# Kernel optimization log

Measured on AMD Instinct MI355X. Metric: run time of the kernel, lower is better.

Reference implementation:

```python
import jax, jax.numpy as jnp
import numpy as np
from jax import lax

DN = ('NCHW', 'OIHW', 'NCHW')

def conv(x, w, groups=1):
    return lax.conv_general_dilated(x, w, (1, 1), 'SAME',
                                    feature_group_count=groups,
                                    dimension_numbers=DN)

def layernorm_cf(x, w, b, eps=1e-6):
    # channels-first LayerNorm over dim=1
    u = x.mean(1, keepdims=True)
    s = ((x - u) ** 2).mean(1, keepdims=True)
    xn = (x - u) / jnp.sqrt(s + eps)
    return w[None, :, None, None] * xn + b[None, :, None, None]

def l2norm(x, eps=1e-12):
    n = jnp.sqrt(jnp.sum(x * x, axis=-1, keepdims=True))
    return x / jnp.maximum(n, eps)

def setup_inputs() -> dict:
    key = jax.random.key(0)
    ks = jax.random.split(key, 16)
    B, C, H, W = 4, 192, 128, 128
    heads = 6
    hidden = int(C * 2.66)  # 510
    s = 0.02
    rn = lambda k, shp: jax.random.normal(k, shp, dtype=jnp.float32) * s
    return {
        'x': jax.random.normal(ks[0], (B, C, H, W), dtype=jnp.float32),
        'ln_w': jnp.ones((C,), jnp.float32),
        'ln_b': jnp.zeros((C,), jnp.float32),
        'temperature': jnp.ones((heads, 1, 1), jnp.float32),
        'q_w': rn(ks[1], (C, C, 1, 1)),
        'q_dw_w': rn(ks[2], (C, 1, 3, 3)),
        'kv_w': rn(ks[3], (2 * C, C, 1, 1)),
        'kv_dw_w': rn(ks[4], (2 * C, 1, 3, 3)),
        'proj_w': rn(ks[5], (C, C, 1, 1)),
        'pos_embed': rn(ks[6], (1, C, 1, 1)),
        'pos_q_w': rn(ks[7], (C, C, 1, 1)),
        'pos_k_w': rn(ks[8], (C, C, 1, 1)),
        'sel_in_w': rn(ks[9], (hidden, C, 3, 3)),
        'sel_dw_w': rn(ks[10], (hidden, 1, 3, 3)),
        'sel_out_w': rn(ks[11], (C, hidden, 3, 3)),
        'alpha': jnp.float32(0.5),
    }

def reference(x, ln_w, ln_b, temperature, q_w, q_dw_w, kv_w, kv_dw_w,
              proj_w, pos_embed, pos_q_w, pos_k_w,
              sel_in_w, sel_dw_w, sel_out_w, alpha):
    b, c, h, w = x.shape
    heads = temperature.shape[0]
    ch = c // heads
    n = h * w

    # --- CFA on norm_x (norm_x == norm_y since both are norm(x)) ---
    norm_x = layernorm_cf(x, ln_w, ln_b)
    q = conv(conv(norm_x, q_w), q_dw_w, groups=c)
    kv = conv(conv(norm_x, kv_w), kv_dw_w, groups=2 * c)
    k, v = jnp.split(kv, 2, axis=1)

    q = q.reshape(b, heads, ch, n)
    k = k.reshape(b, heads, ch, n)
    v = v.reshape(b, heads, ch, n)

    qn = l2norm(q)
    kn = l2norm(k)
    attn = jax.nn.softmax(jnp.einsum('bhcn,bhdn->bhcd', qn, kn) * temperature[None], axis=-1)
    out = jnp.einsum('bhcd,bhdn->bhcn', attn, v)

    pos_x = norm_x + pos_embed
    pos_q = conv(pos_x, pos_q_w).reshape(b, heads, ch, n)
    pos_k = conv(pos_x, pos_k_w).reshape(b, heads, ch, n)
    pos_attn = jax.nn.softmax(jnp.einsum('bhcn,bhdn->bhcd', pos_q, pos_k), axis=-1)
    pos_out = jnp.einsum('bhcd,bhdn->bhcn', pos_attn, v)

    out = (out + pos_out).reshape(b, c, h, w)
    out = conv(out, proj_w)
    x = x + alpha * out

    # --- SEL (conv-FFN) ---
    nx = layernorm_cf(x, ln_w, ln_b)
    g = conv(nx, sel_in_w)
    g = conv(g, sel_dw_w, groups=g.shape[1])
    g = jax.nn.silu(g)
    g = conv(g, sel_out_w)
    x = x + (1.0 - alpha) * g
    return x
```

## Files before the change

kernel.cpp:

```cpp
#include <hip/hip_runtime.h>
#include <hip/hip_bf16.h>
#include <stdint.h>

#define DEVI __device__ __forceinline__

typedef __attribute__((ext_vector_type(8))) unsigned short us8;
typedef __attribute__((ext_vector_type(4))) unsigned short us4;
typedef __attribute__((ext_vector_type(8))) __bf16 bf16x8;
typedef __attribute__((ext_vector_type(4))) float f32x4;

#define BB 4
#define CC 192
#define HH 128
#define NPIX 16384
#define MTOT 65536
#define HEADS 6

DEVI float b2f(unsigned short u){ return __uint_as_float(((unsigned)u)<<16); }
DEVI unsigned short f2b(float f){
  unsigned u = __float_as_uint(f);
  return (unsigned short)((u + 0x7fffu + ((u>>16)&1u)) >> 16);
}

DEVI void gload16(const void* g, void* l){
  __builtin_amdgcn_global_load_lds((const __attribute__((address_space(1))) unsigned int*)g,
                                   (__attribute__((address_space(3))) unsigned int*)l,
                                   16, 0, 0);
}

__global__ __launch_bounds__(256)
void ln1_k(const float* __restrict__ x, const float* __restrict__ lnw,
           const float* __restrict__ lnb, unsigned short* __restrict__ nx)
{
  __shared__ float tile[CC*65];
  __shared__ float stats[64*2];
  int gbase = blockIdx.x * 64;
  int b = gbase >> 14; int n0 = gbase & (NPIX-1);
  for (int idx = threadIdx.x; idx < CC*64; idx += 256){
    int c = idx >> 6, j = idx & 63;
    tile[c*65 + j] = x[((size_t)b*CC + c)*NPIX + n0 + j];
  }
  __syncthreads();
  if (threadIdx.x < 64){
    int j = threadIdx.x;
    float s = 0.f, ss = 0.f;
    for (int c = 0; c < CC; c++){ float v = tile[c*65 + j]; s += v; ss += v*v; }
    float mu = s * (1.f/CC);
    float var = ss * (1.f/CC) - mu*mu;
    stats[j*2] = mu; stats[j*2+1] = rsqrtf(var + 1e-6f);
  }
  __syncthreads();
  for (int idx = threadIdx.x; idx < CC*64; idx += 256){
    int c = idx % CC, j = idx / CC;
    float v = (tile[c*65 + j] - stats[j*2]) * stats[j*2+1] * lnw[c] + lnb[c];
    nx[(size_t)(gbase + j)*CC + c] = f2b(v);
  }
}

__global__ __launch_bounds__(256)
void ln2_k(const float* __restrict__ x2, const float* __restrict__ lnw,
           const float* __restrict__ lnb, unsigned short* __restrict__ nx)
{
  int gm = blockIdx.x*4 + (threadIdx.x >> 6);
  int lane = threadIdx.x & 63;
  const float* row = x2 + (size_t)gm*CC;
  float v0 = row[lane], v1 = row[lane+64], v2 = row[lane+128];
  float s = v0+v1+v2, ss = v0*v0+v1*v1+v2*v2;
  #pragma unroll
  for (int o = 32; o >= 1; o >>= 1){
    s  += __shfl_xor(s,  o);
    ss += __shfl_xor(ss, o);
  }
  float mu = s * (1.f/CC);
  float rstd = rsqrtf(ss*(1.f/CC) - mu*mu + 1e-6f);
  unsigned short* o0 = nx + (size_t)gm*CC;
  o0[lane]     = f2b((v0-mu)*rstd*lnw[lane]     + lnb[lane]);
  o0[lane+64]  = f2b((v1-mu)*rstd*lnw[lane+64]  + lnb[lane+64]);
  o0[lane+128] = f2b((v2-mu)*rstd*lnw[lane+128] + lnb[lane+128]);
}

template<int EPI, int NSLICES>
__global__ __launch_bounds__(512, 2)
void gemm256_k(const unsigned short* __restrict__ A, int strideA,
               const unsigned short* __restrict__ W, int Ktot,
               int NcolsW, int NcolsStore, int outStride, int colBlocks,
               unsigned short* __restrict__ outB,
               const float* __restrict__ res, float* __restrict__ outF,
               const float* __restrict__ alphaP,
               const unsigned short* __restrict__ zerop)
{
  __shared__ unsigned short lds[65536];

  const int tid = threadIdx.x;
  const int l  = tid & 63;
  const int w  = tid >> 6;
  const int wm = w >> 2;
  const int wn = w & 3;

  const int q8 = gridDim.x >> 3;
  const int bid = (blockIdx.x & 7)*q8 + (blockIdx.x >> 3);
  const int mblk = bid / colBlocks;
  const int nblk = bid - mblk*colBlocks;
  const int m0 = mblk*256, co0 = nblk*256;

  int rowT[4], slotX[4];
  #pragma unroll
  for (int i = 0; i < 4; i++){
    rowT[i]  = (w*4 + i)*8 + (l >> 3);
    slotX[i] = (l & 7) ^ (rowT[i] & 7);
  }
  const unsigned short* baseA[4];
  int hhA[4], wwA[4];
  #pragma unroll
  for (int i = 0; i < 4; i++){
    int gm = m0 + rowT[i];
    int np = gm & (NPIX-1);
    hhA[i] = np >> 7; wwA[i] = np & 127;
    baseA[i] = A + (size_t)gm*strideA + (slotX[i] << 3);
  }
  const unsigned short* baseB[4];
  bool bval[4];
  #pragma unroll
  for (int i = 0; i < 4; i++){
    int co = co0 + rowT[i];
    bval[i] = (co < NcolsW);
    baseB[i] = bval[i] ? (W + (size_t)co*Ktot + (slotX[i] << 3)) : (zerop + (l << 3));
  }

  const int NT = Ktot >> 6;

  auto STAGE = [&](int ts){
    int buf = ts & 1;
    unsigned short* la = lds + buf*16384;
    unsigned short* lb = lds + 32768 + buf*16384;
    int ci0, dy = 0, dx = 0;
    if constexpr (NSLICES == 1){ ci0 = ts << 6; }
    else { int cib = ts/9, s = ts - cib*9; ci0 = cib << 6; dy = s/3 - 1; dx = s - (s/3)*3 - 1; }
    #pragma unroll
    for (int i = 0; i < 4; i++){
      const unsigned short* srcA;
      if constexpr (NSLICES == 1){
        srcA = baseA[i] + ci0;
      } else {
        int h2 = hhA[i] + dy, w2 = wwA[i] + dx;
        srcA = ((unsigned)h2 < 128u && (unsigned)w2 < 128u)
             ? (baseA[i] + (dy*HH + dx)*strideA + ci0)
             : (zerop + (l << 3));
      }
      gload16(srcA, la + (w*4 + i)*512);
    }
    #pragma unroll
    for (int i = 0; i < 4; i++){
      const unsigned short* srcB = bval[i] ? (baseB[i] + (ts << 6)) : baseB[i];
      gload16(srcB, lb + (w*4 + i)*512);
    }
  };

  f32x4 acc[8][4] = {};

  STAGE(0);
  for (int t = 0; t < NT; ++t){
    if (t + 1 < NT){
      STAGE(t + 1);
      asm volatile("s_waitcnt vmcnt(8)" ::: "memory");
    } else {
      asm volatile("s_waitcnt vmcnt(0)" ::: "memory");
    }
    __builtin_amdgcn_s_barrier();
    asm volatile("" ::: "memory");
    const unsigned short* la = lds + (t & 1)*16384;
    const unsigned short* lb = lds + 32768 + (t & 1)*16384;
    __builtin_amdgcn_s_setprio(1);
    #pragma unroll
    for (int kk = 0; kk < 2; kk++){
      int ks = kk*4 + (l >> 4);
      bf16x8 bf[4];
      #pragma unroll
      for (int nf = 0; nf < 4; nf++){
        int rb = wn*64 + nf*16 + (l & 15);
        bf[nf] = *(const bf16x8*)(lb + rb*64 + ((ks ^ (rb & 7)) << 3));
      }
      #pragma unroll
      for (int mf = 0; mf < 8; mf++){
        int rm = wm*128 + mf*16 + (l & 15);
        bf16x8 af = *(const bf16x8*)(la + rm*64 + ((ks ^ (rm & 7)) << 3));
        #pragma unroll
        for (int nf = 0; nf < 4; nf++)
          acc[mf][nf] = __builtin_amdgcn_mfma_f32_16x16x32_bf16(af, bf[nf], acc[mf][nf], 0, 0, 0);
      }
    }
    __builtin_amdgcn_s_setprio(0);
    asm volatile("" ::: "memory");
    __builtin_amdgcn_s_barrier();
  }

  float alpha = (EPI == 2) ? (1.f - *alphaP) : 0.f;
  #pragma unroll
  for (int mf = 0; mf < 8; mf++){
    int r0 = m0 + wm*128 + mf*16 + ((l >> 4) << 2);
    #pragma unroll
    for (int nf = 0; nf < 4; nf++){
      int co = co0 + wn*64 + nf*16 + (l & 15);
      if (co < NcolsStore){
        #pragma unroll
        for (int r = 0; r < 4; r++){
          int gm = r0 + r;
          float v = acc[mf][nf][r];
          if constexpr (EPI == 0){
            outB[(size_t)gm*outStride + co] = f2b(v);
          } else {
            int b = gm >> 14, np = gm & (NPIX-1);
            outF[((size_t)b*CC + co)*NPIX + np] = res[(size_t)gm*CC + co] + alpha*v;
          }
        }
      }
    }
  }
}

template<int EPI>
__global__ __launch_bounds__(256, 2)
void gemm_k(const unsigned short* __restrict__ A, int strideA,
            const unsigned short* __restrict__ W, int Ktot,
            int NcolsW, int NcolsStore, int outStride, int colBlocks,
            unsigned short* __restrict__ outB,
            const float* __restrict__ bias,
            const float* __restrict__ res,
            float* __restrict__ outF,
            const float* __restrict__ alphaP,
            const unsigned short* __restrict__ zerop)
{
  __shared__ unsigned short lds[32768];

  const int tid = threadIdx.x;
  const int lane = tid & 63;
  const int wv = tid >> 6;
  const int q8 = gridDim.x >> 3;
  const int bid = (blockIdx.x & 7)*q8 + (blockIdx.x >> 3);
  const int mblk = bid / colBlocks;
  const int nblk = bid - mblk*colBlocks;
  const int m0 = mblk*128, co0 = nblk*128;

  int rowT[4], slotX[4];
  const unsigned short *baseA[4], *baseB[4];
  bool bval[4];
  #pragma unroll
  for (int i = 0; i < 4; i++){
    rowT[i]  = wv*32 + i*8 + (lane >> 3);
    slotX[i] = (lane & 7) ^ (rowT[i] & 7);
    baseA[i] = A + (size_t)(m0 + rowT[i])*strideA + (slotX[i] << 3);
    int co = co0 + rowT[i];
    bval[i] = (co < NcolsW);
    baseB[i] = bval[i] ? (W + (size_t)co*Ktot + (slotX[i] << 3)) : (zerop + (lane << 3));
  }

  const int NT = Ktot >> 6;

  auto STAGE = [&](int ts){
    unsigned short* la = lds + (ts & 1)*16384;
    #pragma unroll
    for (int i = 0; i < 4; i++)
      gload16(baseA[i] + (ts << 6), (char*)la + (wv*4 + i)*1024);
    #pragma unroll
    for (int i = 0; i < 4; i++)
      gload16(bval[i] ? (baseB[i] + (ts << 6)) : baseB[i],
              (char*)la + 16384 + (wv*4 + i)*1024);
  };

  f32x4 acc[4][4] = {};

  STAGE(0);
  for (int t = 0; t < NT; ++t){
    if (t + 1 < NT){
      STAGE(t + 1);
      asm volatile("s_waitcnt vmcnt(8)" ::: "memory");
    } else {
      asm volatile("s_waitcnt vmcnt(0)" ::: "memory");
    }
    __builtin_amdgcn_s_barrier();
    asm volatile("" ::: "memory");
    const unsigned short* la = lds + (t & 1)*16384;
    const unsigned short* lb = la + 8192;
    __builtin_amdgcn_s_setprio(1);
    #pragma unroll
    for (int kk = 0; kk < 2; kk++){
      int ks = kk*4 + (lane >> 4);
      bf16x8 af[4], bfr[4];
      #pragma unroll
      for (int mi = 0; mi < 4; mi++){
        int rm = (wv >> 1)*64 + mi*16 + (lane & 15);
        af[mi] = *(const bf16x8*)(la + rm*64 + ((ks ^ (rm & 7)) << 3));
      }
      #pragma unroll
      for (int ni = 0; ni < 4; ni++){
        int rb = (wv & 1)*64 + ni*16 + (lane & 15);
        bfr[ni] = *(const bf16x8*)(lb + rb*64 + ((ks ^ (rb & 7)) << 3));
      }
      #pragma unroll
      for (int mi = 0; mi < 4; mi++)
        #pragma unroll
        for (int ni = 0; ni < 4; ni++)
          acc[mi][ni] = __builtin_amdgcn_mfma_f32_16x16x32_bf16(af[mi], bfr[ni], acc[mi][ni], 0, 0, 0);
    }
    __builtin_amdgcn_s_setprio(0);
    asm volatile("" ::: "memory");
    __builtin_amdgcn_s_barrier();
  }

  float alpha = 0.f;
  if (EPI == 1) alpha = *alphaP;
  const int colb = co0 + (wv & 1)*64;
  const int rowb = m0 + (wv >> 1)*64;
  #pragma unroll
  for (int mi = 0; mi < 4; mi++){
    int r0 = rowb + mi*16 + ((lane >> 4) << 2);
    #pragma unroll
    for (int ni = 0; ni < 4; ni++){
      int co = colb + ni*16 + (lane & 15);
      if (co < NcolsStore){
        float bv = (EPI == 0 && bias) ? bias[co] : 0.f;
        #pragma unroll
        for (int r = 0; r < 4; r++){
          int gm = r0 + r;
          float v = acc[mi][ni][r];
          if constexpr (EPI == 0){
            outB[(size_t)gm*outStride + co] = f2b(v + bv);
          } else {
            int b = gm >> 14, np = gm & (NPIX-1);
            outF[(size_t)gm*CC + co] = res[((size_t)b*CC + co)*NPIX + np] + alpha*v;
          }
        }
      }
    }
  }
}

template<int NCHV, int DOSILU>
__global__ __launch_bounds__(256)
void dw_k(const unsigned short* __restrict__ src, int strideS,
          const float* __restrict__ wtT, int wstride,
          unsigned short* __restrict__ dst, int strideD)
{
  const int q8 = gridDim.x >> 3;
  const int bid = (blockIdx.x & 7)*q8 + (blockIdx.x >> 3);
  int idx = bid*256 + threadIdx.x;
  int gm = idx / NCHV;
  int cb = idx - gm*NCHV;
  int c = cb*8;
  int np = gm & (NPIX-1);
  int hh = np >> 7, ww = np & 127;
  float acc[8] = {0,0,0,0,0,0,0,0};
  #pragma unroll
  for (int s = 0; s < 9; s++){
    int dy = s/3 - 1, dx = s%3 - 1;
    int h2 = hh + dy, w2 = ww + dx;
    if ((unsigned)h2 < 128u && (unsigned)w2 < 128u){
      us8 t = *(const us8*)(src + (size_t)(gm + dy*HH + dx)*strideS + c);
      f32x4 w0 = *(const f32x4*)(wtT + s*wstride + c);
      f32x4 w1 = *(const f32x4*)(wtT + s*wstride + c + 4);
      #pragma unroll
      for (int j = 0; j < 4; j++){
        acc[j]   += b2f(t[j])   * w0[j];
        acc[4+j] += b2f(t[4+j]) * w1[j];
      }
    }
  }
  us8 o;
  #pragma unroll
  for (int j = 0; j < 8; j++){
    float v = acc[j];
    if (DOSILU) v = v / (1.f + __expf(-v));
    o[j] = f2b(v);
  }
  *(us8*)(dst + (size_t)gm*strideD + c) = o;
}

__global__ __launch_bounds__(192)
void sumsq_k(const unsigned short* __restrict__ q, int stride, float* __restrict__ part)
{
  int b = blockIdx.x >> 5, ch = blockIdx.x & 31;
  int c = threadIdx.x;
  const unsigned short* base = q + ((size_t)b*NPIX + ch*512)*stride + c;
  float acc = 0.f;
  for (int r = 0; r < 512; r++){ float v = b2f(base[(size_t)r*stride]); acc += v*v; }
  part[(size_t)(b*32 + ch)*CC + c] = acc;
}

__global__ __launch_bounds__(256)
void pairdot_k(const unsigned short* __restrict__ qb, const unsigned short* __restrict__ kb,
               int stride, float* __restrict__ Spart)
{
  __shared__ unsigned short qt[4096];
  __shared__ unsigned short kt[4096];
  __shared__ float part[4][32][32];
  int bh = blockIdx.x >> 3, chunk = blockIdx.x & 7;
  int b = bh / HEADS, h = bh - b*HEADS;
  int t = threadIdx.x;
  int w = t >> 6, l = t & 63;
  int c4 = l >> 3, d4 = l & 7;
  size_t gm0 = (size_t)b*NPIX + (size_t)chunk*2048;
  int srow = t >> 2, scol = (t & 3) << 3;
  float acc[4][4] = {};
  for (int sub = 0; sub < 16; sub++){
    __syncthreads();
    #pragma unroll
    for (int hh2 = 0; hh2 < 2; hh2++){
      size_t gr = gm0 + sub*128 + hh2*64 + srow;
      us8 vq = *(const us8*)(qb + gr*stride + h*32 + scol);
      us8 vk = *(const us8*)(kb + gr*stride + h*32 + scol);
      *(us8*)(qt + hh2*2048 + t*8) = vq;
      *(us8*)(kt + hh2*2048 + t*8) = vk;
    }
    __syncthreads();
    #pragma unroll 4
    for (int nn = 0; nn < 32; nn++){
      int n = w*32 + nn;
      us4 qv = *(const us4*)(qt + n*32 + c4*4);
      us4 kv = *(const us4*)(kt + n*32 + d4*4);
      float qf[4], kf[4];
      #pragma unroll
      for (int i = 0; i < 4; i++){ qf[i] = b2f(qv[i]); kf[i] = b2f(kv[i]); }
      #pragma unroll
      for (int i = 0; i < 4; i++)
        #pragma unroll
        for (int j = 0; j < 4; j++)
          acc[i][j] += qf[i]*kf[j];
    }
  }
  __syncthreads();
  #pragma unroll
  for (int i = 0; i < 4; i++)
    #pragma unroll
    for (int j = 0; j < 4; j++)
      part[w][c4*4 + i][d4*4 + j] = acc[i][j];
  __syncthreads();
  #pragma unroll
  for (int o = t; o < 1024; o += 256){
    int c = o >> 5, d = o & 31;
    Spart[(size_t)blockIdx.x*1024 + o] =
      part[0][c][d] + part[1][c][d] + part[2][c][d] + part[3][c][d];
  }
}

__global__ __launch_bounds__(64)
void smax_k(const float* __restrict__ Spos, const float* __restrict__ Scfa,
            const float* __restrict__ qnp, const float* __restrict__ knp,
            const float* __restrict__ temp, float* __restrict__ att)
{
  int bh = blockIdx.x; int b = bh / HEADS, h = bh - b*HEADS;
  __shared__ float kn[32];
  int t = threadIdx.x;
  if (t < 32){
    float ss = 0.f;
    for (int ck = 0; ck < 32; ck++) ss += knp[((size_t)b*32 + ck)*CC + h*32 + t];
    kn[t] = fmaxf(sqrtf(ss), 1e-12f);
  }
  __syncthreads();
  if (t >= 32) return;
  int c = t;
  float ssq = 0.f;
  for (int ck = 0; ck < 32; ck++) ssq += qnp[((size_t)b*32 + ck)*CC + h*32 + c];
  float qn = fmaxf(sqrtf(ssq), 1e-12f);
  float rowS[32], rowP[32];
  #pragma unroll
  for (int d = 0; d < 32; d++){
    float sv = 0.f, pv = 0.f;
    for (int ck = 0; ck < 8; ck++){
      sv += Scfa[(size_t)(bh*8 + ck)*1024 + c*32 + d];
      pv += Spos[(size_t)(bh*8 + ck)*1024 + c*32 + d];
    }
    rowS[d] = sv; rowP[d] = pv;
  }
  float tv = temp[h];
  float m1 = -3e38f, m2 = -3e38f;
  #pragma unroll
  for (int d = 0; d < 32; d++){
    rowS[d] = rowS[d] / (qn*kn[d]) * tv;
    m1 = fmaxf(m1, rowS[d]);
    m2 = fmaxf(m2, rowP[d]);
  }
  float s1 = 0.f, s2 = 0.f;
  #pragma unroll
  for (int d = 0; d < 32; d++){
    rowS[d] = __expf(rowS[d] - m1); s1 += rowS[d];
    rowP[d] = __expf(rowP[d] - m2); s2 += rowP[d];
  }
  float r1 = 1.f/s1, r2 = 1.f/s2;
  #pragma unroll
  for (int d = 0; d < 32; d++)
    att[(size_t)bh*1024 + c*32 + d] = rowS[d]*r1 + rowP[d]*r2;
}

__global__ __launch_bounds__(256)
void pv_k(const float* __restrict__ att, const unsigned short* __restrict__ vd, int stride,
          unsigned short* __restrict__ outT)
{
  __shared__ float As[32][33];
  int bh = blockIdx.x >> 8; int mc = blockIdx.x & 255;
  int b = bh / HEADS, h = bh - b*HEADS;
  int t = threadIdx.x;
  for (int i = t; i < 1024; i += 256) As[i >> 5][i & 31] = att[(size_t)bh*1024 + i];
  __syncthreads();
  int gm = b*NPIX + mc*64 + (t >> 2);
  int cq = t & 3;
  const unsigned short* vp = vd + (size_t)gm*stride + h*32;
  float acc[8] = {0,0,0,0,0,0,0,0};
  for (int d = 0; d < 32; d++){
    float vv = b2f(vp[d]);
    #pragma unroll
    for (int j = 0; j < 8; j++) acc[j] += As[cq*8 + j][d] * vv;
  }
  us8 o;
  #pragma unroll
  for (int j = 0; j < 8; j++) o[j] = f2b(acc[j]);
  *(us8*)(outT + (size_t)gm*CC + h*32 + cq*8) = o;
}

__global__ void castcopy_k(const float* __restrict__ s, unsigned short* __restrict__ d, int n){
  int i = blockIdx.x*256 + threadIdx.x; if (i < n) d[i] = f2b(s[i]);
}
__global__ void prepselin_k(const float* __restrict__ s, unsigned short* __restrict__ d){
  int i = blockIdx.x*256 + threadIdx.x;
  if (i >= 510*1728) return;
  int co = i / 1728, rem = i - co*1728;
  int chunk = rem >> 6, e = rem & 63;
  int cib = chunk / 9, sl = chunk - cib*9;
  int ci = cib*64 + e;
  d[i] = f2b(s[(size_t)(co*192 + ci)*9 + sl]);
}
__global__ void prepselout_k(const float* __restrict__ s, unsigned short* __restrict__ d){
  int i = blockIdx.x*256 + threadIdx.x;
  if (i >= 192*4608) return;
  int co = i / 4608, rem = i - co*4608;
  int chunk = rem >> 6, e = rem & 63;
  int cib = chunk / 9, sl = chunk - cib*9;
  int ci = cib*64 + e;
  d[i] = (ci < 510) ? f2b(s[(size_t)(co*510 + ci)*9 + sl]) : (unsigned short)0;
}
__global__ void prepbias_k(const float* __restrict__ pq, const float* __restrict__ pk,
                           const float* __restrict__ pe, float* __restrict__ bias){
  int r = blockIdx.x*64 + threadIdx.x;
  if (r >= 960) return;
  float s = 0.f;
  if (r < 384){
    const float* Wp = (r < 192) ? pq : pk;
    int co = (r < 192) ? r : r - 192;
    for (int ci = 0; ci < 192; ci++) s += Wp[co*192 + ci]*pe[ci];
  }
  bias[r] = s;
}
__global__ void prepdwT_k(const float* __restrict__ qdw, const float* __restrict__ kvdw,
                          const float* __restrict__ seldw,
                          float* __restrict__ wqkv, float* __restrict__ wsel){
  int i = blockIdx.x*256 + threadIdx.x;
  if (i < 9*576){
    int s = i / 576, c = i - s*576;
    wqkv[i] = (c < 192) ? qdw[c*9 + s] : kvdw[(size_t)(c-192)*9 + s];
  }
  int j = i - 9*576;
  if (j >= 0 && j < 9*512){
    int s = j / 512, c = j - s*512;
    wsel[j] = (c < 510) ? seldw[(size_t)c*9 + s] : 0.f;
  }
}

extern "C" void kernel_launch(void* const* d_in, const int* in_sizes, int n_in,
                              void* d_out, int out_size, void* d_ws, size_t ws_size,
                              hipStream_t stream)
{
  const float* x       = (const float*)d_in[0];
  const float* ln_w    = (const float*)d_in[1];
  const float* ln_b    = (const float*)d_in[2];
  const float* temp    = (const float*)d_in[3];
  const float* q_w     = (const float*)d_in[4];
  const float* q_dw    = (const float*)d_in[5];
  const float* kv_w    = (const float*)d_in[6];
  const float* kv_dw   = (const float*)d_in[7];
  const float* proj_w  = (const float*)d_in[8];
  const float* pos_e   = (const float*)d_in[9];
  const float* posq_w  = (const float*)d_in[10];
  const float* posk_w  = (const float*)d_in[11];
  const float* selin_w = (const float*)d_in[12];
  const float* seldw_w = (const float*)d_in[13];
  const float* selout_w= (const float*)d_in[14];
  const float* alphaP  = (const float*)d_in[15];

  char* ws = (char*)d_ws;
  unsigned short* zerop  = (unsigned short*)(ws + 0);
  float* biasC           = (float*)(ws + 4096);
  float* Spos            = (float*)(ws + 8192);
  float* Scfa            = (float*)(ws + 794624);
  float* qnp             = (float*)(ws + 1581056);
  float* knp             = (float*)(ws + 1679360);
  float* att             = (float*)(ws + 1777664);
  unsigned short* WC     = (unsigned short*)(ws + 2097152);
  unsigned short* Wproj  = (unsigned short*)(ws + 2465792);
  unsigned short* Wselin = (unsigned short*)(ws + 2539520);
  unsigned short* Wselout= (unsigned short*)(ws + 4302080);
  float* WdwQKV          = (float*)(ws + 6071552);
  float* WdwSEL          = (float*)(ws + 6092288);
  unsigned short* normx  = (unsigned short*)(ws + 8388608);
  unsigned short* outT   = normx;
  unsigned short* qp     = (unsigned short*)(ws + 33554432);
  float*          x2     = (float*)(ws + 33554432);
  unsigned short* nx     = (unsigned short*)(ws + 83886080);
  unsigned short* g2     = (unsigned short*)(ws + 83886080);
  unsigned short* qkvd   = (unsigned short*)(ws + 159383552);
  unsigned short* g      = qkvd;

  hipMemsetAsync(zerop, 0, 4096, stream);

  castcopy_k<<<144, 256, 0, stream>>>(posq_w, WC,          36864);
  castcopy_k<<<144, 256, 0, stream>>>(posk_w, WC + 36864,  36864);
  castcopy_k<<<144, 256, 0, stream>>>(q_w,    WC + 73728,  36864);
  castcopy_k<<<288, 256, 0, stream>>>(kv_w,   WC + 110592, 73728);
  castcopy_k<<<144, 256, 0, stream>>>(proj_w, Wproj,       36864);
  prepselin_k<<<3443, 256, 0, stream>>>(selin_w, Wselin);
  prepselout_k<<<3456, 256, 0, stream>>>(selout_w, Wselout);
  prepbias_k<<<15, 64, 0, stream>>>(posq_w, posk_w, pos_e, biasC);
  prepdwT_k<<<39, 256, 0, stream>>>(q_dw, kv_dw, seldw_w, WdwQKV, WdwSEL);

  ln1_k<<<1024, 256, 0, stream>>>(x, ln_w, ln_b, normx);
  gemm_k<0><<<512*8, 256, 0, stream>>>(normx, 192, WC, 192, 960, 960, 960, 8,
                                       qp, biasC, nullptr, nullptr, alphaP, zerop);
  pairdot_k<<<192, 256, 0, stream>>>(qp, qp + 192, 960, Spos);
  dw_k<72,0><<<18432, 256, 0, stream>>>(qp + 384, 960, WdwQKV, 576, qkvd, 576);
  sumsq_k<<<128, 192, 0, stream>>>(qkvd,       576, qnp);
  sumsq_k<<<128, 192, 0, stream>>>(qkvd + 192, 576, knp);
  pairdot_k<<<192, 256, 0, stream>>>(qkvd, qkvd + 192, 576, Scfa);
  smax_k<<<24, 64, 0, stream>>>(Spos, Scfa, qnp, knp, temp, att);
  pv_k<<<24*256, 256, 0, stream>>>(att, qkvd + 384, 576, outT);
  gemm_k<1><<<512*2, 256, 0, stream>>>(outT, 192, Wproj, 192, 192, 192, 192, 2,
                                       nullptr, nullptr, x, x2, alphaP, zerop);
  ln2_k<<<16384, 256, 0, stream>>>(x2, ln_w, ln_b, nx);
  gemm256_k<0,9><<<512, 512, 0, stream>>>(nx, 192, Wselin, 1728, 510, 512, 512, 2,
                                          g, nullptr, nullptr, alphaP, zerop);
  dw_k<64,1><<<16384, 256, 0, stream>>>(g, 512, WdwSEL, 512, g2, 512);
  gemm256_k<2,9><<<256, 512, 0, stream>>>(g2, 512, Wselout, 4608, 192, 192, 0, 1,
                                          nullptr, x2, (float*)d_out, alphaP, zerop);
}
```

Baseline: 855.0 us.

## Retile SEL GEMMs, interleave loads with MFMA phases, split QKV outputs, fuse small kernels

The 256-row GEMM kernel is templated on warp layout and tile shape. The sel_out GEMM now uses a 256x192 tile, so it no longer pads N to 256 and wastes MFMA work on unused columns. Next-tile loads are split into four parts that are issued between MFMA phases, with a barrier after each phase. The first GEMM writes the qkv columns into a separate buffer with a 576 stride so the depthwise pass reads them densely. Smaller changes merge the weight-cast kernels and the two sumsq kernels into one launch each, and make pv_k vectorised with V held in registers. The extra barriers per k-step and the full vmcnt(0) wait could reduce overlap in exchange.

```diff
diff --git a/kernel.cpp b/kernel.cpp
--- a/kernel.cpp
+++ b/kernel.cpp
@@ -79,7 +79,7 @@
   o0[lane+128] = f2b((v2-mu)*rstd*lnw[lane+128] + lnb[lane+128]);
 }
 
-template<int EPI, int NSLICES>
+template<int EPI, int NSLICES, int WM, int WN, int MF, int NF, int NB>
 __global__ __launch_bounds__(512, 2)
 void gemm256_k(const unsigned short* __restrict__ A, int strideA,
                const unsigned short* __restrict__ W, int Ktot,
@@ -89,118 +89,125 @@
                const float* __restrict__ alphaP,
                const unsigned short* __restrict__ zerop)
 {
-  __shared__ unsigned short lds[65536];
+  constexpr int BN = WN*NF*16;
+  __shared__ unsigned short lds[2*256*64 + 2*BN*64];
 
   const int tid = threadIdx.x;
   const int l  = tid & 63;
   const int w  = tid >> 6;
-  const int wm = w >> 2;
-  const int wn = w & 3;
+  const int wm = w / WN;
+  const int wn = w % WN;
 
   const int q8 = gridDim.x >> 3;
   const int bid = (blockIdx.x & 7)*q8 + (blockIdx.x >> 3);
   const int mblk = bid / colBlocks;
   const int nblk = bid - mblk*colBlocks;
-  const int m0 = mblk*256, co0 = nblk*256;
-
-  int rowT[4], slotX[4];
+  const int m0 = mblk*256, co0 = nblk*BN;
+
+  int rowA[4], slotA[4], hhA[4], wwA[4];
+  const unsigned short* baseA[4];
   #pragma unroll
   for (int i = 0; i < 4; i++){
-    rowT[i]  = (w*4 + i)*8 + (l >> 3);
-    slotX[i] = (l & 7) ^ (rowT[i] & 7);
-  }
-  const unsigned short* baseA[4];
-  int hhA[4], wwA[4];
-  #pragma unroll
-  for (int i = 0; i < 4; i++){
-    int gm = m0 + rowT[i];
+    rowA[i]  = (w*4 + i)*8 + (l >> 3);
+    slotA[i] = (l & 7) ^ (rowA[i] & 7);
+    int gm = m0 + rowA[i];
     int np = gm & (NPIX-1);
     hhA[i] = np >> 7; wwA[i] = np & 127;
-    baseA[i] = A + (size_t)gm*strideA + (slotX[i] << 3);
-  }
-  const unsigned short* baseB[4];
-  bool bval[4];
-  #pragma unroll
-  for (int i = 0; i < 4; i++){
-    int co = co0 + rowT[i];
+    baseA[i] = A + (size_t)gm*strideA + (slotA[i] << 3);
+  }
+  const unsigned short* baseB[NB];
+  bool bval[NB];
+  #pragma unroll
+  for (int i = 0; i < NB; i++){
+    int rowB = (w*NB + i)*8 + (l >> 3);
+    int slot = (l & 7) ^ (rowB & 7);
+    int co = co0 + rowB;
     bval[i] = (co < NcolsW);
-    baseB[i] = bval[i] ? (W + (size_t)co*Ktot + (slotX[i] << 3)) : (zerop + (l << 3));
+    baseB[i] = bval[i] ? (W + (size_t)co*Ktot + (slot << 3)) : (zerop + (l << 3));
   }
 
   const int NT = Ktot >> 6;
 
-  auto STAGE = [&](int ts){
-    int buf = ts & 1;
-    unsigned short* la = lds + buf*16384;
-    unsigned short* lb = lds + 32768 + buf*16384;
+  auto STAGE_PART = [&](int ts, int p){
+    unsigned short* la = lds + (ts & 1)*16384;
+    unsigned short* lb = lds + 32768 + (ts & 1)*(BN*64);
     int ci0, dy = 0, dx = 0;
-    if constexpr (NSLICES == 1){ ci0 = ts << 6; }
-    else { int cib = ts/9, s = ts - cib*9; ci0 = cib << 6; dy = s/3 - 1; dx = s - (s/3)*3 - 1; }
-    #pragma unroll
-    for (int i = 0; i < 4; i++){
-      const unsigned short* srcA;
-      if constexpr (NSLICES == 1){
-        srcA = baseA[i] + ci0;
-      } else {
-        int h2 = hhA[i] + dy, w2 = wwA[i] + dx;
-        srcA = ((unsigned)h2 < 128u && (unsigned)w2 < 128u)
-             ? (baseA[i] + (dy*HH + dx)*strideA + ci0)
-             : (zerop + (l << 3));
-      }
-      gload16(srcA, la + (w*4 + i)*512);
-    }
-    #pragma unroll
-    for (int i = 0; i < 4; i++){
-      const unsigned short* srcB = bval[i] ? (baseB[i] + (ts << 6)) : baseB[i];
-      gload16(srcB, lb + (w*4 + i)*512);
+    if constexpr (NSLICES == 9){
+      int cib = ts/9, s = ts - cib*9; ci0 = cib << 6; dy = s/3 - 1; dx = s - (s/3)*3 - 1;
+    } else { ci0 = ts << 6; }
+    if (p < 2){
+      #pragma unroll
+      for (int ii = 0; ii < 2; ii++){
+        int i = p*2 + ii;
+        const unsigned short* srcA;
+        if constexpr (NSLICES == 9){
+          int h2 = hhA[i] + dy, w2 = wwA[i] + dx;
+          srcA = ((unsigned)h2 < 128u && (unsigned)w2 < 128u)
+               ? (baseA[i] + (dy*HH + dx)*strideA + ci0)
+               : (zerop + (l << 3));
+        } else {
+          srcA = baseA[i] + ci0;
+        }
+        gload16(srcA, la + (w*4 + i)*512);
+      }
+    } else if (p == 2){
+      #pragma unroll
+      for (int i = 0; i < 2; i++)
+        gload16(bval[i] ? (baseB[i] + (ts << 6)) : baseB[i], lb + (w*NB + i)*512);
+    } else {
+      #pragma unroll
+      for (int i = 2; i < NB; i++)
+        gload16(bval[i] ? (baseB[i] + (ts << 6)) : baseB[i], lb + (w*NB + i)*512);
     }
   };
 
-  f32x4 acc[8][4] = {};
-
-  STAGE(0);
+  f32x4 acc[MF][NF] = {};
+
+  #pragma unroll
+  for (int p = 0; p < 4; p++) STAGE_PART(0, p);
+
   for (int t = 0; t < NT; ++t){
-    if (t + 1 < NT){
-      STAGE(t + 1);
-      asm volatile("s_waitcnt vmcnt(8)" ::: "memory");
-    } else {
-      asm volatile("s_waitcnt vmcnt(0)" ::: "memory");
-    }
+    asm volatile("s_waitcnt vmcnt(0)" ::: "memory");
     __builtin_amdgcn_s_barrier();
     asm volatile("" ::: "memory");
     const unsigned short* la = lds + (t & 1)*16384;
-    const unsigned short* lb = lds + 32768 + (t & 1)*16384;
-    __builtin_amdgcn_s_setprio(1);
-    #pragma unroll
-    for (int kk = 0; kk < 2; kk++){
-      int ks = kk*4 + (l >> 4);
-      bf16x8 bf[4];
-      #pragma unroll
-      for (int nf = 0; nf < 4; nf++){
-        int rb = wn*64 + nf*16 + (l & 15);
-        bf[nf] = *(const bf16x8*)(lb + rb*64 + ((ks ^ (rb & 7)) << 3));
-      }
-      #pragma unroll
-      for (int mf = 0; mf < 8; mf++){
-        int rm = wm*128 + mf*16 + (l & 15);
+    const unsigned short* lb = lds + 32768 + (t & 1)*(BN*64);
+    bf16x8 bfr[NF];
+    #pragma unroll
+    for (int ph = 0; ph < 4; ph++){
+      const int kk = ph >> 1, mh = ph & 1;
+      if (t + 1 < NT) STAGE_PART(t + 1, ph);
+      const int ks = kk*4 + (l >> 4);
+      if (mh == 0){
+        #pragma unroll
+        for (int nf = 0; nf < NF; nf++){
+          int rb = wn*(NF*16) + nf*16 + (l & 15);
+          bfr[nf] = *(const bf16x8*)(lb + rb*64 + ((ks ^ (rb & 7)) << 3));
+        }
+      }
+      __builtin_amdgcn_s_setprio(1);
+      #pragma unroll
+      for (int mi = 0; mi < MF/2; mi++){
+        int mf = mh*(MF/2) + mi;
+        int rm = wm*(MF*16) + mf*16 + (l & 15);
         bf16x8 af = *(const bf16x8*)(la + rm*64 + ((ks ^ (rm & 7)) << 3));
         #pragma unroll
-        for (int nf = 0; nf < 4; nf++)
-          acc[mf][nf] = __builtin_amdgcn_mfma_f32_16x16x32_bf16(af, bf[nf], acc[mf][nf], 0, 0, 0);
-      }
-    }
-    __builtin_amdgcn_s_setprio(0);
-    asm volatile("" ::: "memory");
-    __builtin_amdgcn_s_barrier();
+        for (int nf = 0; nf < NF; nf++)
+          acc[mf][nf] = __builtin_amdgcn_mfma_f32_16x16x32_bf16(af, bfr[nf], acc[mf][nf], 0, 0, 0);
+      }
+      __builtin_amdgcn_s_setprio(0);
+      asm volatile("" ::: "memory");
+      if (ph < 3){ __builtin_amdgcn_s_barrier(); asm volatile("" ::: "memory"); }
+    }
   }
 
   float alpha = (EPI == 2) ? (1.f - *alphaP) : 0.f;
   #pragma unroll
-  for (int mf = 0; mf < 8; mf++){
-    int r0 = m0 + wm*128 + mf*16 + ((l >> 4) << 2);
-    #pragma unroll
-    for (int nf = 0; nf < 4; nf++){
-      int co = co0 + wn*64 + nf*16 + (l & 15);
+  for (int mf = 0; mf < MF; mf++){
+    int r0 = m0 + wm*(MF*16) + mf*16 + ((l >> 4) << 2);
+    #pragma unroll
+    for (int nf = 0; nf < NF; nf++){
+      int co = co0 + wn*(NF*16) + nf*16 + (l & 15);
       if (co < NcolsStore){
         #pragma unroll
         for (int r = 0; r < 4; r++){
@@ -224,6 +231,7 @@
             const unsigned short* __restrict__ W, int Ktot,
             int NcolsW, int NcolsStore, int outStride, int colBlocks,
             unsigned short* __restrict__ outB,
+            unsigned short* __restrict__ outB2,
             const float* __restrict__ bias,
             const float* __restrict__ res,
             float* __restrict__ outF,
@@ -309,6 +317,9 @@
 
   float alpha = 0.f;
   if (EPI == 1) alpha = *alphaP;
+  unsigned short* dstB = outB;
+  int dstStr = outStride, coAdj = 0;
+  if (EPI == 0 && outB2 && co0 >= 384){ dstB = outB2; dstStr = 576; coAdj = 384; }
   const int colb = co0 + (wv & 1)*64;
   const int rowb = m0 + (wv >> 1)*64;
   #pragma unroll
@@ -324,7 +335,7 @@
           int gm = r0 + r;
           float v = acc[mi][ni][r];
           if constexpr (EPI == 0){
-            outB[(size_t)gm*outStride + co] = f2b(v + bv);
+            dstB[(size_t)gm*dstStr + (co - coAdj)] = f2b(v + bv);
           } else {
             int b = gm >> 14, np = gm & (NPIX-1);
             outF[(size_t)gm*CC + co] = res[((size_t)b*CC + co)*NPIX + np] + alpha*v;
@@ -376,14 +387,16 @@
 }
 
 __global__ __launch_bounds__(192)
-void sumsq_k(const unsigned short* __restrict__ q, int stride, float* __restrict__ part)
-{
-  int b = blockIdx.x >> 5, ch = blockIdx.x & 31;
+void sumsq2_k(const unsigned short* __restrict__ qkvd, float* __restrict__ qnp,
+              float* __restrict__ knp)
+{
+  int which = blockIdx.x >> 7;
+  int b = (blockIdx.x >> 5) & 3, ch = blockIdx.x & 31;
   int c = threadIdx.x;
-  const unsigned short* base = q + ((size_t)b*NPIX + ch*512)*stride + c;
+  const unsigned short* base = qkvd + which*192 + ((size_t)b*NPIX + ch*512)*576 + c;
   float acc = 0.f;
-  for (int r = 0; r < 512; r++){ float v = b2f(base[(size_t)r*stride]); acc += v*v; }
-  part[(size_t)(b*32 + ch)*CC + c] = acc;
+  for (int r = 0; r < 512; r++){ float v = b2f(base[(size_t)r*576]); acc += v*v; }
+  (which ? knp : qnp)[(size_t)(b*32 + ch)*CC + c] = acc;
 }
 
 __global__ __launch_bounds__(256)
@@ -495,20 +508,35 @@
 void pv_k(const float* __restrict__ att, const unsigned short* __restrict__ vd, int stride,
           unsigned short* __restrict__ outT)
 {
-  __shared__ float As[32][33];
+  __shared__ float At[32][36];
   int bh = blockIdx.x >> 8; int mc = blockIdx.x & 255;
   int b = bh / HEADS, h = bh - b*HEADS;
   int t = threadIdx.x;
-  for (int i = t; i < 1024; i += 256) As[i >> 5][i & 31] = att[(size_t)bh*1024 + i];
+  for (int i = t; i < 1024; i += 256){
+    int c = i >> 5, d = i & 31;
+    At[d][c] = att[(size_t)bh*1024 + i];
+  }
   __syncthreads();
   int gm = b*NPIX + mc*64 + (t >> 2);
   int cq = t & 3;
   const unsigned short* vp = vd + (size_t)gm*stride + h*32;
+  float vf[32];
+  #pragma unroll
+  for (int q8i = 0; q8i < 4; q8i++){
+    us8 vv = *(const us8*)(vp + q8i*8);
+    #pragma unroll
+    for (int j = 0; j < 8; j++) vf[q8i*8 + j] = b2f(vv[j]);
+  }
   float acc[8] = {0,0,0,0,0,0,0,0};
+  #pragma unroll 8
   for (int d = 0; d < 32; d++){
-    float vv = b2f(vp[d]);
-    #pragma unroll
-    for (int j = 0; j < 8; j++) acc[j] += As[cq*8 + j][d] * vv;
+    f32x4 a0 = *(const f32x4*)&At[d][cq*8];
+    f32x4 a1 = *(const f32x4*)&At[d][cq*8 + 4];
+    #pragma unroll
+    for (int j = 0; j < 4; j++){
+      acc[j]   += a0[j]*vf[d];
+      acc[4+j] += a1[j]*vf[d];
+    }
   }
   us8 o;
   #pragma unroll
@@ -516,8 +544,16 @@
   *(us8*)(outT + (size_t)gm*CC + h*32 + cq*8) = o;
 }
 
-__global__ void castcopy_k(const float* __restrict__ s, unsigned short* __restrict__ d, int n){
-  int i = blockIdx.x*256 + threadIdx.x; if (i < n) d[i] = f2b(s[i]);
+__global__ void prepw_k(const float* __restrict__ pq, const float* __restrict__ pk,
+                        const float* __restrict__ qw, const float* __restrict__ kvw,
+                        const float* __restrict__ pjw,
+                        unsigned short* __restrict__ WC, unsigned short* __restrict__ Wproj){
+  int i = blockIdx.x*256 + threadIdx.x;
+  if (i < 36864)       WC[i] = f2b(pq[i]);
+  else if (i < 73728)  WC[i] = f2b(pk[i - 36864]);
+  else if (i < 110592) WC[i] = f2b(qw[i - 73728]);
+  else if (i < 184320) WC[i] = f2b(kvw[i - 110592]);
+  else if (i < 221184) Wproj[i - 184320] = f2b(pjw[i - 184320]);
 }
 __global__ void prepselin_k(const float* __restrict__ s, unsigned short* __restrict__ d){
   int i = blockIdx.x*256 + threadIdx.x;
@@ -601,41 +637,37 @@
   float* WdwSEL          = (float*)(ws + 6092288);
   unsigned short* normx  = (unsigned short*)(ws + 8388608);
   unsigned short* outT   = normx;
-  unsigned short* qp     = (unsigned short*)(ws + 33554432);
+  unsigned short* qpos   = (unsigned short*)(ws + 33554432);
   float*          x2     = (float*)(ws + 33554432);
+  unsigned short* qkvsep = (unsigned short*)(ws + 83886080);
   unsigned short* nx     = (unsigned short*)(ws + 83886080);
-  unsigned short* g2     = (unsigned short*)(ws + 83886080);
-  unsigned short* qkvd   = (unsigned short*)(ws + 159383552);
+  unsigned short* g2     = (unsigned short*)(ws + 117440512);
+  unsigned short* qkvd   = (unsigned short*)(ws + 184549376);
   unsigned short* g      = qkvd;
 
   hipMemsetAsync(zerop, 0, 4096, stream);
 
-  castcopy_k<<<144, 256, 0, stream>>>(posq_w, WC,          36864);
-  castcopy_k<<<144, 256, 0, stream>>>(posk_w, WC + 36864,  36864);
-  castcopy_k<<<144, 256, 0, stream>>>(q_w,    WC + 73728,  36864);
-  castcopy_k<<<288, 256, 0, stream>>>(kv_w,   WC + 110592, 73728);
-  castcopy_k<<<144, 256, 0, stream>>>(proj_w, Wproj,       36864);
+  prepw_k<<<864, 256, 0, stream>>>(posq_w, posk_w, q_w, kv_w, proj_w, WC, Wproj);
   prepselin_k<<<3443, 256, 0, stream>>>(selin_w, Wselin);
   prepselout_k<<<3456, 256, 0, stream>>>(selout_w, Wselout);
   prepbias_k<<<15, 64, 0, stream>>>(posq_w, posk_w, pos_e, biasC);
   prepdwT_k<<<39, 256, 0, stream>>>(q_dw, kv_dw, seldw_w, WdwQKV, WdwSEL);
 
   ln1_k<<<1024, 256, 0, stream>>>(x, ln_w, ln_b, normx);
-  gemm_k<0><<<512*8, 256, 0, stream>>>(normx, 192, WC, 192, 960, 960, 960, 8,
-                                       qp, biasC, nullptr, nullptr, alphaP, zerop);
-  pairdot_k<<<192, 256, 0, stream>>>(qp, qp + 192, 960, Spos);
-  dw_k<72,0><<<18432, 256, 0, stream>>>(qp + 384, 960, WdwQKV, 576, qkvd, 576);
-  sumsq_k<<<128, 192, 0, stream>>>(qkvd,       576, qnp);
-  sumsq_k<<<128, 192, 0, stream>>>(qkvd + 192, 576, knp);
+  gemm_k<0><<<512*8, 256, 0, stream>>>(normx, 192, WC, 192, 960, 960, 384, 8,
+                                       qpos, qkvsep, biasC, nullptr, nullptr, alphaP, zerop);
+  pairdot_k<<<192, 256, 0, stream>>>(qpos, qpos + 192, 384, Spos);
+  dw_k<72,0><<<18432, 256, 0, stream>>>(qkvsep, 576, WdwQKV, 576, qkvd, 576);
+  sumsq2_k<<<256, 192, 0, stream>>>(qkvd, qnp, knp);
   pairdot_k<<<192, 256, 0, stream>>>(qkvd, qkvd + 192, 576, Scfa);
   smax_k<<<24, 64, 0, stream>>>(Spos, Scfa, qnp, knp, temp, att);
   pv_k<<<24*256, 256, 0, stream>>>(att, qkvd + 384, 576, outT);
   gemm_k<1><<<512*2, 256, 0, stream>>>(outT, 192, Wproj, 192, 192, 192, 192, 2,
-                                       nullptr, nullptr, x, x2, alphaP, zerop);
+                                       nullptr, nullptr, nullptr, x, x2, alphaP, zerop);
   ln2_k<<<16384, 256, 0, stream>>>(x2, ln_w, ln_b, nx);
-  gemm256_k<0,9><<<512, 512, 0, stream>>>(nx, 192, Wselin, 1728, 510, 512, 512, 2,
-                                          g, nullptr, nullptr, alphaP, zerop);
+  gemm256_k<0,9, 2,4, 8,4, 4><<<512, 512, 0, stream>>>(nx, 192, Wselin, 1728, 510, 512, 512, 2,
+                                                       g, nullptr, nullptr, alphaP, zerop);
   dw_k<64,1><<<16384, 256, 0, stream>>>(g, 512, WdwSEL, 512, g2, 512);
-  gemm256_k<2,9><<<256, 512, 0, stream>>>(g2, 512, Wselout, 4608, 192, 192, 0, 1,
-                                          nullptr, x2, (float*)d_out, alphaP, zerop);
-}
+  gemm256_k<2,9, 4,2, 4,6, 3><<<256, 512, 0, stream>>>(g2, 512, Wselout, 4608, 192, 192, 0, 1,
+                                                       nullptr, x2, (float*)d_out, alphaP, zerop);
+}
```

After: 805.8 us. -5.8%, faster.
